# Optimization experiments

Measured on AMD Instinct MI355X. Metric: run time of the kernel, lower is better.

Reference implementation:

```python
import jax, jax.numpy as jnp
import numpy as np
import math

B, S, H, D = 1, 4096, 16, 64
SM_SCALE = 1.0 / math.sqrt(D)

def setup_inputs() -> dict:
    key = jax.random.key(0)
    kq, kk, kv = jax.random.split(key, 3)
    return {
        "query": jax.random.normal(kq, (B, S, H, D), dtype=jnp.float32),
        "key": jax.random.normal(kk, (B, S, H, D), dtype=jnp.float32),
        "value": jax.random.normal(kv, (B, S, H, D), dtype=jnp.float32),
    }

def reference(query, key, value):
    # Module transposes [B,S,H,D] -> [B,H,S,D]; S=4096 is already a multiple of
    # 128 so padding / segment-id masking is a no-op. Backend is non-causal
    # flash attention with sm_scale = 1/sqrt(D); equivalent dense math:
    # scores: [B,H,Sq,Sk]
    scores = jnp.einsum("bqhd,bkhd->bhqk", query, key) * SM_SCALE
    probs = jax.nn.softmax(scores, axis=-1)
    out = jnp.einsum("bhqk,bkhd->bqhd", probs, value)
    return out  # [B,S,H,D]
```

## Files before the change

kernel.cpp:

```cpp
#include <hip/hip_runtime.h>
#include <stdint.h>

#define H_ 16
#define S_ 4096
#define D_ 64
#define ROWSTRIDE (H_ * D_)
#define BK 64
#define NT (S_ / BK)
#define TILE_USH (BK * D_)
#define NBUF 4
#define BUF_USH (2 * TILE_USH)
#define QB 256
#define LP 72
#define LK 72
#define QSCALE (0.125f * 1.44269504088896340736f)
#define LOG2E 1.44269504088896340736f
#define SM_SCALE 0.125f

typedef unsigned short ushort_t;
typedef __attribute__((ext_vector_type(8))) __bf16 bf16x8;
typedef __attribute__((ext_vector_type(16))) float floatx16;
typedef __attribute__((ext_vector_type(8))) unsigned short ushortx8;
typedef __attribute__((ext_vector_type(4))) unsigned short ushortx4;

#if __has_builtin(__builtin_amdgcn_exp2f)
#define EXP2F(x) __builtin_amdgcn_exp2f(x)
#else
#define EXP2F(x) exp2f(x)
#endif

__device__ inline unsigned short f2bf(float x) {
    union { float f; unsigned int u; } c; c.f = x;
    unsigned int r = c.u + 0x7fffu + ((c.u >> 16) & 1u);
    return (unsigned short)(r >> 16);
}
__device__ inline uint32_t cvt_pk_bf16(float a, float b) {
#if __has_builtin(__builtin_amdgcn_cvt_pk_bf16_f32)
    auto r = __builtin_amdgcn_cvt_pk_bf16_f32(a, b);
    uint32_t u; __builtin_memcpy(&u, &r, 4); return u;
#else
    return (uint32_t)f2bf(a) | ((uint32_t)f2bf(b) << 16);
#endif
}
__device__ inline void permswap(uint32_t& a, uint32_t& b, int g2) {
#if __has_builtin(__builtin_amdgcn_permlane32_swap)
    auto r = __builtin_amdgcn_permlane32_swap(a, b, false, false);
    uint32_t tmp[2]; __builtin_memcpy(tmp, &r, 8);
    a = tmp[0]; b = tmp[1];
#else
    uint32_t ra = (uint32_t)__shfl_xor((int)a, 32, 64);
    uint32_t rb = (uint32_t)__shfl_xor((int)b, 32, 64);
    uint32_t na = g2 ? rb : a;
    uint32_t nb = g2 ? b : ra;
    a = na; b = nb;
#endif
}
__device__ inline bf16x8 as_bf16x8(ushortx8 v) {
    union { ushortx8 s; bf16x8 b; } c; c.s = v; return c.b;
}
__device__ inline bf16x8 bf16x8_from_u32(uint32_t a, uint32_t b, uint32_t c, uint32_t d) {
    union { uint32_t u[4]; bf16x8 b; } x; x.u[0]=a; x.u[1]=b; x.u[2]=c; x.u[3]=d; return x.b;
}
__device__ inline void glds16(const void* g, void* l) {
    __builtin_amdgcn_global_load_lds(
        (const __attribute__((address_space(1))) void*)g,
        (__attribute__((address_space(3))) void*)l, 16, 0, 0);
}

__global__ __launch_bounds__(256)
void pack_kv(const float* __restrict__ K, const float* __restrict__ V,
             ushort_t* __restrict__ Kp, ushort_t* __restrict__ Vp) {
    __shared__ ushort_t lT[D_ * 88];
    const int tid = threadIdx.x;
    const int h = blockIdx.x & (H_ - 1);
    const int tile = blockIdx.x >> 4;
    ushort_t* kout = Kp + (size_t)(h * NT + tile) * TILE_USH;
    ushort_t* vout = Vp + (size_t)(h * NT + tile) * TILE_USH;

    #pragma unroll
    for (int p = 0; p < 2; ++p) {
        int idx = tid + p * 256;
        int f = idx >> 6;
        int lo = idx & 63;
        int mk = f >> 2, c = f & 3;
        int l31 = lo & 31, g2 = lo >> 5;
        const float* kp = K + (size_t)(tile * BK + mk * 32 + l31) * ROWSTRIDE + h * D_ + (2 * c + g2) * 8;
        float4 a = *(const float4*)kp;
        float4 b = *(const float4*)(kp + 4);
        ushortx8 u;
        u[0] = f2bf(a.x); u[1] = f2bf(a.y); u[2] = f2bf(a.z); u[3] = f2bf(a.w);
        u[4] = f2bf(b.x); u[5] = f2bf(b.y); u[6] = f2bf(b.z); u[7] = f2bf(b.w);
        *(ushortx8*)&kout[f * 512 + lo * 8] = u;
    }

    #pragma unroll
    for (int p = 0; p < 4; ++p) {
        int idx = tid + p * 256;
        int row = idx >> 4;
        int d4 = (idx & 15) * 4;
        const float* vp = V + (size_t)(tile * BK + row) * ROWSTRIDE + h * D_ + d4;
        float4 vv = *(const float4*)vp;
        lT[(d4 + 0) * 88 + row] = f2bf(vv.x);
        lT[(d4 + 1) * 88 + row] = f2bf(vv.y);
        lT[(d4 + 2) * 88 + row] = f2bf(vv.z);
        lT[(d4 + 3) * 88 + row] = f2bf(vv.w);
    }
    __syncthreads();
    #pragma unroll
    for (int p = 0; p < 2; ++p) {
        int idx = tid + p * 256;
        int f = idx >> 6;
        int lo = idx & 63;
        int md = f >> 2, kc = f & 3;
        int l31 = lo & 31, g2 = lo >> 5;
        ushortx8 u = *(ushortx8*)&lT[(md * 32 + l31) * 88 + (2 * kc + g2) * 8];
        *(ushortx8*)&vout[f * 512 + lo * 8] = u;
    }
}

__global__ __launch_bounds__(320)
void usp_attn_fa8(const float* __restrict__ Q, const ushort_t* __restrict__ Kp,
                  const ushort_t* __restrict__ Vp, float* __restrict__ O) {
    __shared__ __attribute__((aligned(16))) ushort_t smem[NBUF * BUF_USH];
    __shared__ int flags[8];

    const int tid = threadIdx.x;
    const int lane = tid & 63;
    const int wv = tid >> 6;
    const int h = blockIdx.x & (H_ - 1);
    const int qi = blockIdx.x >> 4;
    const int l31 = lane & 31;
    const int g2 = lane >> 5;

    if (tid < 8) flags[tid] = 0;
    __syncthreads();

    const ushort_t* kbase = Kp + (size_t)h * NT * TILE_USH;
    const ushort_t* vbase = Vp + (size_t)h * NT * TILE_USH;

    if (wv == 4) {
        for (int t = 0; t < NT; ++t) {
            if (t >= NBUF) {
                for (;;) {
                    int m0 = __hip_atomic_load(&flags[4], __ATOMIC_ACQUIRE, __HIP_MEMORY_SCOPE_WORKGROUP);
                    int m1 = __hip_atomic_load(&flags[5], __ATOMIC_ACQUIRE, __HIP_MEMORY_SCOPE_WORKGROUP);
                    int m2 = __hip_atomic_load(&flags[6], __ATOMIC_ACQUIRE, __HIP_MEMORY_SCOPE_WORKGROUP);
                    int m3 = __hip_atomic_load(&flags[7], __ATOMIC_ACQUIRE, __HIP_MEMORY_SCOPE_WORKGROUP);
                    if (min(min(m0, m1), min(m2, m3)) >= t - (NBUF - 1)) break;
                    __builtin_amdgcn_s_sleep(1);
                }
            }
            const ushort_t* gK = kbase + (size_t)t * TILE_USH;
            const ushort_t* gV = vbase + (size_t)t * TILE_USH;
            ushort_t* bK = smem + (t & (NBUF - 1)) * BUF_USH;
            ushort_t* bV = bK + TILE_USH;
            #pragma unroll
            for (int i = 0; i < 8; ++i) {
                glds16(gK + i * 512 + lane * 8, bK + i * 512);
                glds16(gV + i * 512 + lane * 8, bV + i * 512);
            }
            __builtin_amdgcn_s_waitcnt(0x0f70);
            __hip_atomic_store(&flags[0], t + 1, __ATOMIC_RELEASE, __HIP_MEMORY_SCOPE_WORKGROUP);
        }
        return;
    }

    const int q0 = qi * QB + wv * 64;

    bf16x8 qf[2][4];
    #pragma unroll
    for (int qh = 0; qh < 2; ++qh) {
        const float* qp = Q + (size_t)(q0 + qh * 32 + l31) * ROWSTRIDE + h * D_ + g2 * 8;
        #pragma unroll
        for (int c = 0; c < 4; ++c) {
            const float4 v0 = *(const float4*)(qp + c * 16);
            const float4 v1 = *(const float4*)(qp + c * 16 + 4);
            qf[qh][c] = bf16x8_from_u32(
                cvt_pk_bf16(v0.x * QSCALE, v0.y * QSCALE),
                cvt_pk_bf16(v0.z * QSCALE, v0.w * QSCALE),
                cvt_pk_bf16(v1.x * QSCALE, v1.y * QSCALE),
                cvt_pk_bf16(v1.z * QSCALE, v1.w * QSCALE));
        }
    }

    floatx16 o[2][2] = {{{0,0,0,0,0,0,0,0,0,0,0,0,0,0,0,0},
                         {0,0,0,0,0,0,0,0,0,0,0,0,0,0,0,0}},
                        {{0,0,0,0,0,0,0,0,0,0,0,0,0,0,0,0},
                         {0,0,0,0,0,0,0,0,0,0,0,0,0,0,0,0}}};
    float rs[2] = {0.f, 0.f};

    for (int t = 0; t < NT; ++t) {
        while (__hip_atomic_load(&flags[0], __ATOMIC_ACQUIRE, __HIP_MEMORY_SCOPE_WORKGROUP) < t + 1)
            __builtin_amdgcn_s_sleep(1);
        const ushortx8* fp = (const ushortx8*)(smem + (t & (NBUF - 1)) * BUF_USH) + lane;

        bf16x8 ab[8];
        #pragma unroll
        for (int f = 0; f < 8; ++f) ab[f] = as_bf16x8(fp[f * 64]);

        floatx16 st[2][2];
        #pragma unroll
        for (int qh = 0; qh < 2; ++qh) {
            #pragma unroll
            for (int mk = 0; mk < 2; ++mk) {
                floatx16 acc = {0,0,0,0,0,0,0,0,0,0,0,0,0,0,0,0};
                #pragma unroll
                for (int c = 0; c < 4; ++c)
                    acc = __builtin_amdgcn_mfma_f32_32x32x16_bf16(ab[mk * 4 + c], qf[qh][c], acc, 0, 0, 0);
                st[qh][mk] = acc;
            }
        }

        uint32_t qd[2][2][8];
        #pragma unroll
        for (int qh = 0; qh < 2; ++qh) {
            #pragma unroll
            for (int mk = 0; mk < 2; ++mk) {
                #pragma unroll
                for (int i = 0; i < 8; ++i) {
                    float p0 = EXP2F(st[qh][mk][2 * i]);
                    float p1 = EXP2F(st[qh][mk][2 * i + 1]);
                    rs[qh] += p0 + p1;
                    qd[qh][mk][i] = cvt_pk_bf16(p0, p1);
                }
            }
        }

        #pragma unroll
        for (int f = 0; f < 8; ++f) ab[f] = as_bf16x8(fp[512 + f * 64]);

        #pragma unroll
        for (int kc = 0; kc < 4; ++kc) {
            int mk = kc >> 1, ci = kc & 1;
            #pragma unroll
            for (int qh = 0; qh < 2; ++qh) {
                uint32_t a0 = qd[qh][mk][ci * 4 + 0], a1 = qd[qh][mk][ci * 4 + 1];
                uint32_t b0 = qd[qh][mk][ci * 4 + 2], b1 = qd[qh][mk][ci * 4 + 3];
                permswap(a0, b0, g2);
                permswap(a1, b1, g2);
                bf16x8 pf = bf16x8_from_u32(a0, a1, b0, b1);
                #pragma unroll
                for (int md = 0; md < 2; ++md)
                    o[qh][md] = __builtin_amdgcn_mfma_f32_32x32x16_bf16(ab[md * 4 + kc], pf, o[qh][md], 0, 0, 0);
            }
        }

        __hip_atomic_store(&flags[4 + wv], t + 1, __ATOMIC_RELEASE, __HIP_MEMORY_SCOPE_WORKGROUP);
    }

    #pragma unroll
    for (int qh = 0; qh < 2; ++qh) {
        float r = rs[qh];
        r += __shfl_xor(r, 32, 64);
        float inv = 1.f / r;
        float* op = O + (size_t)(q0 + qh * 32 + l31) * ROWSTRIDE + h * D_;
        #pragma unroll
        for (int md = 0; md < 2; ++md) {
            #pragma unroll
            for (int rq = 0; rq < 4; ++rq) {
                int d0 = md * 32 + rq * 8 + 4 * g2;
                float4 w;
                w.x = o[qh][md][4 * rq + 0] * inv;
                w.y = o[qh][md][4 * rq + 1] * inv;
                w.z = o[qh][md][4 * rq + 2] * inv;
                w.w = o[qh][md][4 * rq + 3] * inv;
                *(float4*)&op[d0] = w;
            }
        }
    }
}

__global__ __launch_bounds__(256, 2)
void usp_attn_fa(const float* __restrict__ Q, const float* __restrict__ K,
                 const float* __restrict__ V, float* __restrict__ O) {
    __shared__ unsigned short fK[BK * LK];
    __shared__ unsigned short fVT[D_ * LK];
    __shared__ unsigned short fP[4 * 16 * LP];
    const int tid = threadIdx.x;
    const int lane = tid & 63;
    const int wv = tid >> 6;
    const int h = blockIdx.x & (H_ - 1);
    const int qt = blockIdx.x >> 4;
    const int q0 = qt * 64 + wv * 16;
    const int m16 = lane & 15;
    const int g = lane >> 4;
    typedef __attribute__((ext_vector_type(4))) float f4;
    bf16x8 qf[2];
    {
        const float* qp = Q + (size_t)(q0 + m16) * ROWSTRIDE + h * D_ + g * 8;
        for (int c = 0; c < 2; ++c) {
            ushortx8 u;
            #pragma unroll
            for (int j = 0; j < 8; ++j) u[j] = f2bf(qp[c * 32 + j]);
            qf[c] = as_bf16x8(u);
        }
    }
    f4 o[4] = {{0,0,0,0},{0,0,0,0},{0,0,0,0},{0,0,0,0}};
    float mrow[4] = {-1e30f,-1e30f,-1e30f,-1e30f};
    float lrow[4] = {0.f,0.f,0.f,0.f};
    unsigned short* myP = &fP[wv * 16 * LP];
    for (int k0 = 0; k0 < S_; k0 += BK) {
        __syncthreads();
        #pragma unroll
        for (int p = 0; p < 4; ++p) {
            int idx = tid + p * 256;
            int row = idx >> 4;
            int c4 = (idx & 15) * 4;
            const float* kp = K + (size_t)(k0 + row) * ROWSTRIDE + h * D_ + c4;
            float4 kv = *(const float4*)kp;
            ushortx4 ku;
            ku[0] = f2bf(kv.x); ku[1] = f2bf(kv.y); ku[2] = f2bf(kv.z); ku[3] = f2bf(kv.w);
            *(ushortx4*)&fK[row * LK + c4] = ku;
            const float* vp = V + (size_t)(k0 + row) * ROWSTRIDE + h * D_ + c4;
            float4 vv = *(const float4*)vp;
            fVT[(c4 + 0) * LK + row] = f2bf(vv.x);
            fVT[(c4 + 1) * LK + row] = f2bf(vv.y);
            fVT[(c4 + 2) * LK + row] = f2bf(vv.z);
            fVT[(c4 + 3) * LK + row] = f2bf(vv.w);
        }
        __syncthreads();
        f4 s[4];
        #pragma unroll
        for (int t = 0; t < 4; ++t) {
            f4 acc = {0,0,0,0};
            #pragma unroll
            for (int c = 0; c < 2; ++c) {
                bf16x8 kf = as_bf16x8(*(ushortx8*)&fK[(t * 16 + m16) * LK + c * 32 + g * 8]);
                acc = __builtin_amdgcn_mfma_f32_16x16x32_bf16(qf[c], kf, acc, 0, 0, 0);
            }
            s[t] = acc * SM_SCALE;
        }
        float mnew[4], rsum[4];
        #pragma unroll
        for (int r = 0; r < 4; ++r) {
            float pm = fmaxf(fmaxf(s[0][r], s[1][r]), fmaxf(s[2][r], s[3][r]));
            #pragma unroll
            for (int msk = 1; msk <= 8; msk <<= 1) pm = fmaxf(pm, __shfl_xor(pm, msk, 64));
            mnew[r] = fmaxf(mrow[r], pm);
            rsum[r] = 0.f;
        }
        #pragma unroll
        for (int t = 0; t < 4; ++t) {
            #pragma unroll
            for (int r = 0; r < 4; ++r) {
                float p = EXP2F((s[t][r] - mnew[r]) * LOG2E);
                rsum[r] += p;
                myP[(g * 4 + r) * LP + t * 16 + m16] = f2bf(p);
            }
        }
        #pragma unroll
        for (int r = 0; r < 4; ++r) {
            #pragma unroll
            for (int msk = 1; msk <= 8; msk <<= 1) rsum[r] += __shfl_xor(rsum[r], msk, 64);
            float alpha = EXP2F((mrow[r] - mnew[r]) * LOG2E);
            lrow[r] = lrow[r] * alpha + rsum[r];
            mrow[r] = mnew[r];
            o[0][r] *= alpha; o[1][r] *= alpha; o[2][r] *= alpha; o[3][r] *= alpha;
        }
        #pragma unroll
        for (int c = 0; c < 2; ++c) {
            bf16x8 pf = as_bf16x8(*(ushortx8*)&myP[m16 * LP + c * 32 + g * 8]);
            #pragma unroll
            for (int t = 0; t < 4; ++t) {
                bf16x8 vf = as_bf16x8(*(ushortx8*)&fVT[(t * 16 + m16) * LK + c * 32 + g * 8]);
                o[t] = __builtin_amdgcn_mfma_f32_16x16x32_bf16(pf, vf, o[t], 0, 0, 0);
            }
        }
    }
    float* op = O + (size_t)q0 * ROWSTRIDE + h * D_;
    #pragma unroll
    for (int r = 0; r < 4; ++r) {
        float inv = 1.f / lrow[r];
        int row = g * 4 + r;
        #pragma unroll
        for (int t = 0; t < 4; ++t)
            op[(size_t)row * ROWSTRIDE + t * 16 + m16] = o[t][r] * inv;
    }
}

extern "C" void kernel_launch(void* const* d_in, const int* in_sizes, int n_in,
                              void* d_out, int out_size, void* d_ws, size_t ws_size,
                              hipStream_t stream) {
    const float* Q = (const float*)d_in[0];
    const float* K = (const float*)d_in[1];
    const float* V = (const float*)d_in[2];
    float* O = (float*)d_out;
    const size_t packed = (size_t)H_ * NT * TILE_USH;
    const size_t packed_bytes = 2 * packed * sizeof(ushort_t);
    if (ws_size >= packed_bytes) {
        ushort_t* Kp = (ushort_t*)d_ws;
        ushort_t* Vp = Kp + packed;
        pack_kv<<<dim3(H_ * NT), dim3(256), 0, stream>>>(K, V, Kp, Vp);
        usp_attn_fa8<<<dim3(H_ * (S_ / QB)), dim3(320), 0, stream>>>(Q, Kp, Vp, O);
    } else {
        usp_attn_fa<<<dim3(H_ * (S_ / 64)), dim3(256), 0, stream>>>(Q, K, V, O);
    }
}
```

Measured before the change: 172.8 us.

## Load packed K/V tiles directly from global memory, dropping LDS producer warp

Removes the dedicated producer wavefront, the 4-stage LDS ring buffer and the flag-based spin synchronisation. Each compute wave now reads its packed K and V fragments straight from global memory (through L2/L1) into registers every iteration. This cuts LDS traffic, atomic polling and the extra warp, but each of the four waves now fetches the same tiles redundantly and load latency is no longer hidden by an asynchronous prefetcher.

```diff
diff --git a/kernel.cpp b/kernel.cpp
--- a/kernel.cpp
+++ b/kernel.cpp
@@ -8,8 +8,6 @@
 #define BK 64
 #define NT (S_ / BK)
 #define TILE_USH (BK * D_)
-#define NBUF 4
-#define BUF_USH (2 * TILE_USH)
 #define QB 256
 #define LP 72
 #define LK 72
@@ -60,11 +58,6 @@
 }
 __device__ inline bf16x8 bf16x8_from_u32(uint32_t a, uint32_t b, uint32_t c, uint32_t d) {
     union { uint32_t u[4]; bf16x8 b; } x; x.u[0]=a; x.u[1]=b; x.u[2]=c; x.u[3]=d; return x.b;
-}
-__device__ inline void glds16(const void* g, void* l) {
-    __builtin_amdgcn_global_load_lds(
-        (const __attribute__((address_space(1))) void*)g,
-        (__attribute__((address_space(3))) void*)l, 16, 0, 0);
 }
 
 __global__ __launch_bounds__(256)
@@ -118,12 +111,9 @@
     }
 }
 
-__global__ __launch_bounds__(320)
+__global__ __launch_bounds__(256)
 void usp_attn_fa8(const float* __restrict__ Q, const ushort_t* __restrict__ Kp,
                   const ushort_t* __restrict__ Vp, float* __restrict__ O) {
-    __shared__ __attribute__((aligned(16))) ushort_t smem[NBUF * BUF_USH];
-    __shared__ int flags[8];
-
     const int tid = threadIdx.x;
     const int lane = tid & 63;
     const int wv = tid >> 6;
@@ -132,38 +122,8 @@
     const int l31 = lane & 31;
     const int g2 = lane >> 5;
 
-    if (tid < 8) flags[tid] = 0;
-    __syncthreads();
-
-    const ushort_t* kbase = Kp + (size_t)h * NT * TILE_USH;
-    const ushort_t* vbase = Vp + (size_t)h * NT * TILE_USH;
-
-    if (wv == 4) {
-        for (int t = 0; t < NT; ++t) {
-            if (t >= NBUF) {
-                for (;;) {
-                    int m0 = __hip_atomic_load(&flags[4], __ATOMIC_ACQUIRE, __HIP_MEMORY_SCOPE_WORKGROUP);
-                    int m1 = __hip_atomic_load(&flags[5], __ATOMIC_ACQUIRE, __HIP_MEMORY_SCOPE_WORKGROUP);
-                    int m2 = __hip_atomic_load(&flags[6], __ATOMIC_ACQUIRE, __HIP_MEMORY_SCOPE_WORKGROUP);
-                    int m3 = __hip_atomic_load(&flags[7], __ATOMIC_ACQUIRE, __HIP_MEMORY_SCOPE_WORKGROUP);
-                    if (min(min(m0, m1), min(m2, m3)) >= t - (NBUF - 1)) break;
-                    __builtin_amdgcn_s_sleep(1);
-                }
-            }
-            const ushort_t* gK = kbase + (size_t)t * TILE_USH;
-            const ushort_t* gV = vbase + (size_t)t * TILE_USH;
-            ushort_t* bK = smem + (t & (NBUF - 1)) * BUF_USH;
-            ushort_t* bV = bK + TILE_USH;
-            #pragma unroll
-            for (int i = 0; i < 8; ++i) {
-                glds16(gK + i * 512 + lane * 8, bK + i * 512);
-                glds16(gV + i * 512 + lane * 8, bV + i * 512);
-            }
-            __builtin_amdgcn_s_waitcnt(0x0f70);
-            __hip_atomic_store(&flags[0], t + 1, __ATOMIC_RELEASE, __HIP_MEMORY_SCOPE_WORKGROUP);
-        }
-        return;
-    }
+    const ushortx8* kb = (const ushortx8*)Kp + (size_t)h * NT * 512 + lane;
+    const ushortx8* vb = (const ushortx8*)Vp + (size_t)h * NT * 512 + lane;
 
     const int q0 = qi * QB + wv * 64;
 
@@ -190,13 +150,14 @@
     float rs[2] = {0.f, 0.f};
 
     for (int t = 0; t < NT; ++t) {
-        while (__hip_atomic_load(&flags[0], __ATOMIC_ACQUIRE, __HIP_MEMORY_SCOPE_WORKGROUP) < t + 1)
-            __builtin_amdgcn_s_sleep(1);
-        const ushortx8* fp = (const ushortx8*)(smem + (t & (NBUF - 1)) * BUF_USH) + lane;
-
-        bf16x8 ab[8];
-        #pragma unroll
-        for (int f = 0; f < 8; ++f) ab[f] = as_bf16x8(fp[f * 64]);
+        const size_t tb = (size_t)t * 512;
+
+        bf16x8 kk[8];
+        #pragma unroll
+        for (int f = 0; f < 8; ++f) kk[f] = as_bf16x8(kb[tb + f * 64]);
+        bf16x8 vv[8];
+        #pragma unroll
+        for (int f = 0; f < 8; ++f) vv[f] = as_bf16x8(vb[tb + f * 64]);
 
         floatx16 st[2][2];
         #pragma unroll
@@ -206,7 +167,7 @@
                 floatx16 acc = {0,0,0,0,0,0,0,0,0,0,0,0,0,0,0,0};
                 #pragma unroll
                 for (int c = 0; c < 4; ++c)
-                    acc = __builtin_amdgcn_mfma_f32_32x32x16_bf16(ab[mk * 4 + c], qf[qh][c], acc, 0, 0, 0);
+                    acc = __builtin_amdgcn_mfma_f32_32x32x16_bf16(kk[mk * 4 + c], qf[qh][c], acc, 0, 0, 0);
                 st[qh][mk] = acc;
             }
         }
@@ -227,9 +188,6 @@
         }
 
         #pragma unroll
-        for (int f = 0; f < 8; ++f) ab[f] = as_bf16x8(fp[512 + f * 64]);
-
-        #pragma unroll
         for (int kc = 0; kc < 4; ++kc) {
             int mk = kc >> 1, ci = kc & 1;
             #pragma unroll
@@ -241,11 +199,9 @@
                 bf16x8 pf = bf16x8_from_u32(a0, a1, b0, b1);
                 #pragma unroll
                 for (int md = 0; md < 2; ++md)
-                    o[qh][md] = __builtin_amdgcn_mfma_f32_32x32x16_bf16(ab[md * 4 + kc], pf, o[qh][md], 0, 0, 0);
-            }
-        }
-
-        __hip_atomic_store(&flags[4 + wv], t + 1, __ATOMIC_RELEASE, __HIP_MEMORY_SCOPE_WORKGROUP);
+                    o[qh][md] = __builtin_amdgcn_mfma_f32_32x32x16_bf16(vv[md * 4 + kc], pf, o[qh][md], 0, 0, 0);
+            }
+        }
     }
 
     #pragma unroll
@@ -391,7 +347,7 @@
         ushort_t* Kp = (ushort_t*)d_ws;
         ushort_t* Vp = Kp + packed;
         pack_kv<<<dim3(H_ * NT), dim3(256), 0, stream>>>(K, V, Kp, Vp);
-        usp_attn_fa8<<<dim3(H_ * (S_ / QB)), dim3(320), 0, stream>>>(Q, Kp, Vp, O);
+        usp_attn_fa8<<<dim3(H_ * (S_ / QB)), dim3(256), 0, stream>>>(Q, Kp, Vp, O);
     } else {
         usp_attn_fa<<<dim3(H_ * (S_ / 64)), dim3(256), 0, stream>>>(Q, K, V, O);
     }
```

Result: slower. 214.9 us (+24.4%).
